# Kernel tuning notes

Hardware: AMD Instinct MI355X
Metric: run time of the kernel (lower is better)

Reference implementation:

```python
import jax, jax.numpy as jnp
import numpy as np

MATSIZE = 1024
TRIU_LEN = MATSIZE * (MATSIZE + 1) // 2  # 524800
_rows, _cols = np.triu_indices(MATSIZE)
ROWS = jnp.asarray(_rows)
COLS = jnp.asarray(_cols)


def setup_inputs() -> dict:
    key = jax.random.key(0)
    inputs = jax.random.normal(key, (128, TRIU_LEN), dtype=jnp.float32)
    return {"inputs": inputs}


def reference(inputs) -> jnp.ndarray:
    # Scatter each batch vector into the upper triangle of an (M, M) matrix,
    # zeros elsewhere. Vectorized over the batch via a single indexed set.
    B = inputs.shape[0]
    out = jnp.zeros((B, MATSIZE, MATSIZE), dtype=inputs.dtype)
    return out.at[:, ROWS, COLS].set(inputs)
```

## Files before the change

kernel.cpp:

```cpp
#include <hip/hip_runtime.h>


constexpr int M = 1024;
constexpr int BATCH = 128;
constexpr int TRIU_LEN = M * (M + 1) / 2;
constexpr int QUADS_PER_ROW = M / 4;

__global__ __launch_bounds__(256) void triu_scatter_kernel(
    const float* __restrict__ in, float* __restrict__ out) {
    int tid = blockIdx.x * blockDim.x + threadIdx.x;
    int qc = tid & (QUADS_PER_ROW - 1);
    int r  = (tid >> 8) & (M - 1);
    int b  = tid >> 18;
    int c0 = qc << 2;

    int row_base = r * M - (r * (r - 1)) / 2 - r;
    const float* inb = in + (long)b * TRIU_LEN + row_base;

    float4 v;
    if (c0 >= r) {
        v.x = inb[c0];
        v.y = inb[c0 + 1];
        v.z = inb[c0 + 2];
        v.w = inb[c0 + 3];
    } else if (c0 + 3 < r) {
        v = make_float4(0.f, 0.f, 0.f, 0.f);
    } else {
        v.x = (c0     >= r) ? inb[c0]     : 0.f;
        v.y = (c0 + 1 >= r) ? inb[c0 + 1] : 0.f;
        v.z = (c0 + 2 >= r) ? inb[c0 + 2] : 0.f;
        v.w = (c0 + 3 >= r) ? inb[c0 + 3] : 0.f;
    }

    reinterpret_cast<float4*>(out)[tid] = v;
}

extern "C" void kernel_launch(void* const* d_in, const int* in_sizes, int n_in,
                              void* d_out, int out_size, void* d_ws, size_t ws_size,
                              hipStream_t stream) {
    const float* in = (const float*)d_in[0];
    float* out = (float*)d_out;

    const int total_quads = BATCH * M * QUADS_PER_ROW;
    const int block = 256;
    const int grid = total_quads / block;

    triu_scatter_kernel<<<grid, block, 0, stream>>>(in, out);
}
```

Before: 665.6 us.

## Use aligned float4 input loads with realignment and per-row wavefront mapping

Each 64-lane wavefront now handles one output row, and each thread covers four float4 chunks across the row. Unaligned row starts in the packed input are handled by loading aligned float4 pairs and shifting lanes, replacing four scalar loads per output quad. This aims to reduce load instruction count and improve memory efficiency. The aligned hi load may read a few floats past the row end, up to the buffer end on the final row.

```diff
diff --git a/kernel.cpp b/kernel.cpp
--- a/kernel.cpp
+++ b/kernel.cpp
@@ -4,35 +4,47 @@
 constexpr int M = 1024;
 constexpr int BATCH = 128;
 constexpr int TRIU_LEN = M * (M + 1) / 2;
-constexpr int QUADS_PER_ROW = M / 4;
 
-__global__ __launch_bounds__(256) void triu_scatter_kernel(
+__global__ __launch_bounds__(256) void triu_scatter_v2(
     const float* __restrict__ in, float* __restrict__ out) {
-    int tid = blockIdx.x * blockDim.x + threadIdx.x;
-    int qc = tid & (QUADS_PER_ROW - 1);
-    int r  = (tid >> 8) & (M - 1);
-    int b  = tid >> 18;
-    int c0 = qc << 2;
+    int tid  = blockIdx.x * blockDim.x + threadIdx.x;
+    int lane = tid & 63;
+    int r    = (tid >> 6) & (M - 1);
+    int b    = tid >> 16;
 
     int row_base = r * M - (r * (r - 1)) / 2 - r;
-    const float* inb = in + (long)b * TRIU_LEN + row_base;
+    const float* inb = in + (size_t)b * TRIU_LEN;
+    float* outr = out + ((size_t)b * M + r) * M;
 
-    float4 v;
-    if (c0 >= r) {
-        v.x = inb[c0];
-        v.y = inb[c0 + 1];
-        v.z = inb[c0 + 2];
-        v.w = inb[c0 + 3];
-    } else if (c0 + 3 < r) {
-        v = make_float4(0.f, 0.f, 0.f, 0.f);
-    } else {
-        v.x = (c0     >= r) ? inb[c0]     : 0.f;
-        v.y = (c0 + 1 >= r) ? inb[c0 + 1] : 0.f;
-        v.z = (c0 + 2 >= r) ? inb[c0 + 2] : 0.f;
-        v.w = (c0 + 3 >= r) ? inb[c0 + 3] : 0.f;
+    int sh = row_base & 3;
+
+    #pragma unroll
+    for (int j = 0; j < 4; ++j) {
+        int C = (j << 8) + (lane << 2);
+        float4 v;
+        if ((j << 8) >= r) {
+            int idx0 = row_base + C;
+            const float* base = inb + (idx0 - sh);
+            float4 lo = *reinterpret_cast<const float4*>(base);
+            if (sh == 0) {
+                v = lo;
+            } else {
+                float4 hi = *reinterpret_cast<const float4*>(base + 4);
+                if (sh == 1)      v = make_float4(lo.y, lo.z, lo.w, hi.x);
+                else if (sh == 2) v = make_float4(lo.z, lo.w, hi.x, hi.y);
+                else              v = make_float4(lo.w, hi.x, hi.y, hi.z);
+            }
+        } else if ((j << 8) + 255 < r) {
+            v = make_float4(0.f, 0.f, 0.f, 0.f);
+        } else {
+            int idx0 = row_base + C;
+            v.x = (C     >= r) ? inb[idx0]     : 0.f;
+            v.y = (C + 1 >= r) ? inb[idx0 + 1] : 0.f;
+            v.z = (C + 2 >= r) ? inb[idx0 + 2] : 0.f;
+            v.w = (C + 3 >= r) ? inb[idx0 + 3] : 0.f;
+        }
+        *reinterpret_cast<float4*>(outr + C) = v;
     }
-
-    reinterpret_cast<float4*>(out)[tid] = v;
 }
 
 extern "C" void kernel_launch(void* const* d_in, const int* in_sizes, int n_in,
@@ -41,9 +53,9 @@
     const float* in = (const float*)d_in[0];
     float* out = (float*)d_out;
 
-    const int total_quads = BATCH * M * QUADS_PER_ROW;
+    const int total_threads = BATCH * M * 64;
     const int block = 256;
-    const int grid = total_quads / block;
+    const int grid = total_threads / block;
 
-    triu_scatter_kernel<<<grid, block, 0, stream>>>(in, out);
+    triu_scatter_v2<<<grid, block, 0, stream>>>(in, out);
 }
```

Measured after the change: 677.6 us. Within noise of the previous version (+1.8%).
